# Kernel tuning notes

Measured on AMD Instinct MI355X. Metric: run time of the kernel, lower is better.

The kernel has to match this reference:

```python
import jax, jax.numpy as jnp
import numpy as np

N = 300000      # total points
B = 4           # scenes
C_IN = 64
C_OUT = 128
GRID = 0.5      # voxel size
M = 128         # per-axis voxel index bound (10m / 0.5m = 20 << 128); key fits int32
EPS = 1e-5      # BatchNorm eps


def setup_inputs() -> dict:
    key = jax.random.key(0)
    k1, k2, k3 = jax.random.split(key, 3)
    coord = jax.random.uniform(k1, (N, 3), jnp.float32) * 10.0
    feat = jax.random.normal(k2, (N, C_IN), jnp.float32)
    offset = jnp.array([N // 4, N // 2, 3 * N // 4, N], jnp.int32)  # cumulative counts
    W = jax.random.normal(k3, (C_IN, C_OUT), jnp.float32) * 0.05    # fc weight (no bias)
    gamma = jnp.ones((C_OUT,), jnp.float32)
    beta = jnp.zeros((C_OUT,), jnp.float32)
    return {"coord": coord, "feat": feat, "offset": offset, "W": W, "gamma": gamma, "beta": beta}


def reference(coord, feat, offset, W, gamma, beta):
    n = coord.shape[0]
    # offset2batch: point i belongs to scene searchsorted(offset, i, 'right')
    batch = jnp.searchsorted(offset, jnp.arange(n, dtype=offset.dtype), side='right')
    # fc -> BatchNorm1d (training-mode batch stats, biased var) -> ReLU
    x = feat @ W                                    # [n, C_OUT]
    mean = x.mean(axis=0)
    var = x.var(axis=0)
    x = jax.nn.relu(gamma * (x - mean) * jax.lax.rsqrt(var + EPS) + beta)
    # start = per-scene min coordinate (segment_csr min)
    start = jax.ops.segment_min(coord, batch, num_segments=B)      # [B, 3]
    # voxel_grid: integer voxel index per point, hashed injectively with batch id
    v = jnp.floor((coord - start[batch]) / GRID).astype(jnp.int32)  # [n, 3]
    vkey = ((batch.astype(jnp.int32) * M + v[:, 0]) * M + v[:, 1]) * M + v[:, 2]
    # unique(sorted) with inverse/counts; padded to n for static shapes
    uniq, cluster, counts = jnp.unique(vkey, return_inverse=True, return_counts=True,
                                       size=n, fill_value=-1)
    cluster = cluster.reshape(-1)                   # [n] cluster id per point
    # segment mean of coords, segment max of features (padded segments -> 0)
    cnt = jnp.maximum(counts, 1).astype(coord.dtype)
    coord_out = jax.ops.segment_sum(coord, cluster, num_segments=n) / cnt[:, None]
    fmax = jax.ops.segment_max(x, cluster, num_segments=n)
    feat_out = jnp.where(counts[:, None] > 0, fmax, jnp.zeros((), x.dtype))
    # batch id of each cluster (clusters never cross scenes)
    batch_out = jax.ops.segment_min(batch, cluster, num_segments=n)
    return coord_out, feat_out, cluster, counts, batch_out
```

## Files before the change

### kernel.cpp

```cpp
#include <hip/hip_runtime.h>
#include <stdint.h>

#define CIN   64
#define COUT  128
#define EPSB  1e-5f
#define NWORDS2 4096
#define MAXNC 32768
#define STRD  68

typedef short bf16x8 __attribute__((ext_vector_type(8)));
typedef float f32x4  __attribute__((ext_vector_type(4)));

__device__ __forceinline__ int batch_of(int i, const int* __restrict__ off, int B) {
    int b = 0;
    for (int j = 0; j < B - 1; ++j) b += (i >= off[j]) ? 1 : 0;
    return b;
}

__device__ __forceinline__ unsigned enc(float x) {
    unsigned b = __float_as_uint(x);
    return (b & 0x80000000u) ? ~b : (b | 0x80000000u);
}
__device__ __forceinline__ float dec(unsigned u) {
    unsigned b = (u & 0x80000000u) ? (u ^ 0x80000000u) : ~u;
    return __uint_as_float(b);
}

__device__ __forceinline__ unsigned short rne_bf16(float f) {
    unsigned u = __float_as_uint(f);
    unsigned r = u + 0x7FFFu + ((u >> 16) & 1u);
    return (unsigned short)(r >> 16);
}

__global__ void k_init(float* __restrict__ coordOut, float* __restrict__ batchOut, int n,
                       unsigned* __restrict__ pooledU, int* __restrict__ countsWs,
                       unsigned* __restrict__ flags, int* __restrict__ sceneMin, int nScene,
                       const float* __restrict__ W, unsigned short* __restrict__ Wb)
{
    long i = (long)blockIdx.x * blockDim.x + threadIdx.x;
    long stride = (long)gridDim.x * blockDim.x;
    for (long t = i; t < 3L * n; t += stride) coordOut[t] = 0.f;
    for (long t = i; t < n; t += stride) batchOut[t] = 2147483648.0f;
    for (long t = i; t < (long)MAXNC * COUT; t += stride) pooledU[t] = 0u;
    for (long t = i; t < MAXNC; t += stride) countsWs[t] = 0;
    for (long t = i; t < NWORDS2; t += stride) flags[t] = 0u;
    for (long t = i; t < nScene; t += stride) sceneMin[t] = 0x7F800000;
    for (long t = i; t < 32 * 64 * 8; t += stride) {
        int fragIdx = (int)(t >> 9);
        int r = (int)(t & 511);
        int lane = r >> 3, j = r & 7;
        int s  = fragIdx & 1;
        int kt = (fragIdx >> 1) & 1;
        int nt = fragIdx >> 2;
        int k  = kt * 32 + (lane >> 4) * 8 + j;
        int nc = nt * 16 + (lane & 15);
        float w = W[k * COUT + nc];
        unsigned short hi = rne_bf16(w);
        if (s == 0) Wb[t] = hi;
        else {
            float hf = __uint_as_float(((unsigned)hi) << 16);
            Wb[t] = rne_bf16(w - hf);
        }
    }
}

__global__ void k_scene_min(const float* __restrict__ coord, const int* __restrict__ off,
                            int n, int B, int* __restrict__ sceneMin)
{
    __shared__ int smin[12];
    if (threadIdx.x < 3 * B) smin[threadIdx.x] = 0x7F800000;
    __syncthreads();
    int t = blockIdx.x * blockDim.x + threadIdx.x;
    if (t < n) {
        int b = batch_of(t, off, B);
        for (int d = 0; d < 3; ++d)
            atomicMin(&smin[b * 3 + d], __float_as_int(coord[t * 3 + d]));
    }
    __syncthreads();
    if (threadIdx.x < 3 * B) atomicMin(&sceneMin[threadIdx.x], smin[threadIdx.x]);
}

__global__ void k_vkey(const float* __restrict__ coord, const int* __restrict__ off,
                       int n, int B, const int* __restrict__ sceneMin,
                       int* __restrict__ vkeyWs, unsigned* __restrict__ flags)
{
    int t = blockIdx.x * blockDim.x + threadIdx.x;
    if (t >= n) return;
    int b = batch_of(t, off, B);
    int key = b;
    #pragma unroll
    for (int d = 0; d < 3; ++d) {
        float s = __int_as_float(sceneMin[b * 3 + d]);
        int v = (int)floorf((coord[t * 3 + d] - s) * 2.0f);
        key = (key << 5) + v;
    }
    vkeyWs[t] = key;
    atomicOr(&flags[key >> 5], 1u << (key & 31));
}

__global__ void k_scan1(const unsigned* __restrict__ flags,
                        unsigned* __restrict__ wordPrefix, int* __restrict__ dNC)
{
    __shared__ unsigned wsum[16];
    const int t = threadIdx.x, lane = t & 63, wv = t >> 6;
    unsigned loc[4]; unsigned sum = 0;
    #pragma unroll
    for (int e = 0; e < 4; ++e) { loc[e] = (unsigned)__popc(flags[4 * t + e]); sum += loc[e]; }
    unsigned incl = sum;
    #pragma unroll
    for (int d = 1; d < 64; d <<= 1) {
        unsigned u = __shfl_up(incl, d, 64);
        if (lane >= d) incl += u;
    }
    if (lane == 63) wsum[wv] = incl;
    __syncthreads();
    if (wv == 0) {
        unsigned v = (lane < 16) ? wsum[lane] : 0u;
        unsigned iv = v;
        #pragma unroll
        for (int d = 1; d < 16; d <<= 1) {
            unsigned u = __shfl_up(iv, d, 64);
            if (lane >= d) iv += u;
        }
        if (lane < 16) wsum[lane] = iv - v;
    }
    __syncthreads();
    unsigned run = wsum[wv] + incl - sum;
    #pragma unroll
    for (int e = 0; e < 4; ++e) { wordPrefix[4 * t + e] = run; run += loc[e]; }
    if (t == 1023) *dNC = (int)run;
}

__global__ void k_cluster(const int* __restrict__ vkeyWs, const int* __restrict__ off,
                          int n, int B,
                          const unsigned* __restrict__ flags, const unsigned* __restrict__ wordPrefix,
                          float* __restrict__ clusterOut,
                          int* __restrict__ countsWs, float* __restrict__ batchOut)
{
    int t = blockIdx.x * blockDim.x + threadIdx.x;
    if (t >= n) return;
    int key = vkeyWs[t];
    int w = key >> 5, bit = key & 31;
    int c = (int)wordPrefix[w] + __popc(flags[w] & ((1u << bit) - 1u));
    clusterOut[t] = (float)c;
    atomicAdd(&countsWs[c], 1);
    batchOut[c] = (float)(key >> 15);
}

__global__ void k_scan2(const int* __restrict__ counts, int* __restrict__ cursor)
{
    __shared__ int wsum[16];
    const int t = threadIdx.x, lane = t & 63, wv = t >> 6;
    const int base = t * 32;
    int loc[32]; int sum = 0;
    #pragma unroll
    for (int e = 0; e < 32; ++e) { loc[e] = counts[base + e]; sum += loc[e]; }
    int incl = sum;
    #pragma unroll
    for (int d = 1; d < 64; d <<= 1) {
        int u = __shfl_up(incl, d, 64);
        if (lane >= d) incl += u;
    }
    if (lane == 63) wsum[wv] = incl;
    __syncthreads();
    if (wv == 0) {
        int v = (lane < 16) ? wsum[lane] : 0;
        int iv = v;
        #pragma unroll
        for (int d = 1; d < 16; d <<= 1) {
            int u = __shfl_up(iv, d, 64);
            if (lane >= d) iv += u;
        }
        if (lane < 16) wsum[lane] = iv - v;
    }
    __syncthreads();
    int run = wsum[wv] + incl - sum;
    #pragma unroll
    for (int e = 0; e < 32; ++e) { cursor[base + e] = run; run += loc[e]; }
}

__global__ void k_scatter(const float* __restrict__ clusterOut, int n,
                          int* __restrict__ cursor, int* __restrict__ perm,
                          int* __restrict__ sortedCid)
{
    int t = blockIdx.x * blockDim.x + threadIdx.x;
    if (t >= n) return;
    int c = (int)clusterOut[t];
    int pos = atomicAdd(&cursor[c], 1);
    perm[pos] = t;
    sortedCid[pos] = c;
}

__global__ __launch_bounds__(256, 2) void k_fused(
    const float* __restrict__ feat, const float* __restrict__ coord,
    const unsigned short* __restrict__ Wb,
    const int* __restrict__ perm, const int* __restrict__ sortedCid,
    int n, int nWin, int gFused,
    unsigned* __restrict__ pooledU, float* __restrict__ coordOut,
    float* __restrict__ partials)
{
    __shared__ float lds[4][64 * STRD];
    __shared__ float cst[4][192];
    __shared__ float accS[256];
    const int tid = threadIdx.x, wave = tid >> 6, lane = tid & 63;
    accS[tid] = 0.f;
    __syncthreads();

    const int wid = blockIdx.x * 4 + wave;
    const int q = lane >> 4, c16 = lane & 15;

    if (wid < nWin) {
        const int base = wid * 64;
        const int nvalid = min(64, n - base);
        const int pv = (lane < nvalid) ? perm[base + lane] : 0;
        const int cv = (lane < nvalid) ? sortedCid[base + lane] : -1;
        float* st = lds[wave];
        float* cs = cst[wave];

        int prevc = __shfl_up(cv, 1, 64);
        unsigned long long bmask = __ballot(lane > 0 && lane < nvalid && cv != prevc);

        for (int i0 = 0; i0 < 64; i0 += 4) {
            int idx = i0 + q;
            int p = __shfl(pv, idx, 64);
            float4 v = make_float4(0.f, 0.f, 0.f, 0.f);
            if (idx < nvalid)
                v = ((const float4*)(feat + (size_t)p * CIN))[c16];
            *(float4*)&st[idx * STRD + c16 * 4] = v;
        }
        for (int i0 = 0; i0 < 64; i0 += 16) {
            int idx = i0 + (lane >> 2);
            int d = lane & 3;
            int p = __shfl(pv, idx, 64);
            if (d < 3 && idx < nvalid) cs[idx * 3 + d] = coord[p * 3 + d];
        }

        {
            float csum = 0.f;
            int runStart = 0;
            for (int i = 0; i < nvalid; ++i) {
                if (i > 0 && ((bmask >> i) & 1ull)) {
                    int cid = __shfl(cv, i - 1, 64);
                    if (lane < 3) {
                        float* cb = coordOut + (size_t)cid * 3 + lane;
                        if (runStart == 0) atomicAdd(cb, csum);
                        else               *cb = csum;
                    }
                    runStart = i; csum = 0.f;
                }
                if (lane < 3) csum += cs[i * 3 + lane];
            }
            int cidL = __shfl(cv, nvalid - 1, 64);
            if (lane < 3) atomicAdd(coordOut + (size_t)cidL * 3 + lane, csum);
        }

        bf16x8 ahi[4][2], alo[4][2];
        #pragma unroll
        for (int mt = 0; mt < 4; ++mt) {
            #pragma unroll
            for (int kt = 0; kt < 2; ++kt) {
                int m = mt * 16 + c16;
                int k0 = kt * 32 + q * 8;
                float4 fa = *(const float4*)&st[m * STRD + k0];
                float4 fb = *(const float4*)&st[m * STRD + k0 + 4];
                float tmp[8] = { fa.x, fa.y, fa.z, fa.w, fb.x, fb.y, fb.z, fb.w };
                bf16x8 h8, l8;
                #pragma unroll
                for (int j = 0; j < 8; ++j) {
                    unsigned short h = rne_bf16(tmp[j]);
                    float hf = __uint_as_float(((unsigned)h) << 16);
                    h8[j] = (short)h;
                    l8[j] = (short)rne_bf16(tmp[j] - hf);
                }
                ahi[mt][kt] = h8;
                alo[mt][kt] = l8;
            }
        }

        for (int h = 0; h < 2; ++h) {
            bf16x8 bh[4][2], bl[4][2];
            #pragma unroll
            for (int nt2 = 0; nt2 < 4; ++nt2)
                #pragma unroll
                for (int kt = 0; kt < 2; ++kt) {
                    int fi = h * 16 + (nt2 * 2 + kt) * 2;
                    bh[nt2][kt] = *(const bf16x8*)(Wb + ((size_t)fi << 9) + (lane << 3));
                    bl[nt2][kt] = *(const bf16x8*)(Wb + ((size_t)(fi + 1) << 9) + (lane << 3));
                }
            #pragma unroll
            for (int mt = 0; mt < 4; ++mt) {
                #pragma unroll
                for (int nt2 = 0; nt2 < 4; ++nt2) {
                    f32x4 c = {0.f, 0.f, 0.f, 0.f};
                    #pragma unroll
                    for (int kt = 0; kt < 2; ++kt) {
                        c = __builtin_amdgcn_mfma_f32_16x16x32_bf16(alo[mt][kt], bh[nt2][kt], c, 0, 0, 0);
                        c = __builtin_amdgcn_mfma_f32_16x16x32_bf16(ahi[mt][kt], bl[nt2][kt], c, 0, 0, 0);
                        c = __builtin_amdgcn_mfma_f32_16x16x32_bf16(ahi[mt][kt], bh[nt2][kt], c, 0, 0, 0);
                    }
                    int col = nt2 * 16 + c16;
                    int row0 = mt * 16 + q * 4;
                    *(float4*)&st[col * STRD + row0] = make_float4(c[0], c[1], c[2], c[3]);
                }
            }
            float runM = -INFINITY, s1 = 0.f, s2 = 0.f;
            int runStart = 0;
            for (int ip = 0; ip < 16; ++ip) {
                if (ip * 4 >= nvalid) break;
                float4 v = *(const float4*)&st[lane * STRD + ip * 4];
                #pragma unroll
                for (int e = 0; e < 4; ++e) {
                    int i = ip * 4 + e;
                    if (i < nvalid) {
                        if (i > 0 && ((bmask >> i) & 1ull)) {
                            int cid = __shfl(cv, i - 1, 64);
                            unsigned* pb = pooledU + (size_t)cid * COUT + h * 64 + lane;
                            if (runStart == 0) atomicMax(pb, enc(runM));
                            else               *pb = enc(runM);
                            runStart = i;
                            runM = -INFINITY;
                        }
                        float x = (e == 0) ? v.x : (e == 1) ? v.y : (e == 2) ? v.z : v.w;
                        runM = fmaxf(runM, x);
                        s1 += x;
                        s2 = fmaf(x, x, s2);
                    }
                }
            }
            int cidL = __shfl(cv, nvalid - 1, 64);
            atomicMax(pooledU + (size_t)cidL * COUT + h * 64 + lane, enc(runM));
            atomicAdd(&accS[h * 64 + lane],       s1);
            atomicAdd(&accS[128 + h * 64 + lane], s2);
        }
    }

    __syncthreads();
    partials[(size_t)tid * gFused + blockIdx.x] = accS[tid];
}

__global__ void k_redbn(const float* __restrict__ partials, int gFused,
                        const float* __restrict__ gamma, const float* __restrict__ beta,
                        int n, float* __restrict__ scaleShift)
{
    __shared__ float red[512];
    const int j = blockIdx.x;
    const float* colS = partials + (size_t)j * gFused;
    const float* colQ = partials + (size_t)(j + 128) * gFused;
    float s = 0.f, q = 0.f;
    for (int b = threadIdx.x; b < gFused; b += 256) { s += colS[b]; q += colQ[b]; }
    red[threadIdx.x] = s;
    red[256 + threadIdx.x] = q;
    __syncthreads();
    for (int st = 128; st; st >>= 1) {
        if (threadIdx.x < st) {
            red[threadIdx.x] += red[threadIdx.x + st];
            red[256 + threadIdx.x] += red[256 + threadIdx.x + st];
        }
        __syncthreads();
    }
    if (threadIdx.x == 0) {
        float mean = red[0] / (float)n;
        float var  = red[256] / (float)n - mean * mean;
        var = fmaxf(var, 0.f);
        float inv = rsqrtf(var + EPSB);
        float sc = gamma[j] * inv;
        scaleShift[j]        = sc;
        scaleShift[COUT + j] = beta[j] - mean * sc;
    }
}

__global__ void k_final(float* __restrict__ featOut, const unsigned* __restrict__ pooledU,
                        const int* __restrict__ dNC, const float* __restrict__ scaleShift,
                        long featN4, int n,
                        float* __restrict__ coordOut, float* __restrict__ countsOut,
                        const int* __restrict__ countsWs)
{
    long i = (long)blockIdx.x * blockDim.x + threadIdx.x;
    long stride = (long)gridDim.x * blockDim.x;
    long act4 = (long)(*dNC) * (COUT / 4);
    float4* out4 = (float4*)featOut;
    const uint4* p4 = (const uint4*)pooledU;
    for (long idx = i; idx < featN4; idx += stride) {
        float4 v = make_float4(0.f, 0.f, 0.f, 0.f);
        if (idx < act4) {
            int j = (int)((idx * 4) & (COUT - 1));
            uint4 u = p4[idx];
            v.x = fmaxf(fmaf(scaleShift[j + 0], dec(u.x), scaleShift[COUT + j + 0]), 0.f);
            v.y = fmaxf(fmaf(scaleShift[j + 1], dec(u.y), scaleShift[COUT + j + 1]), 0.f);
            v.z = fmaxf(fmaf(scaleShift[j + 2], dec(u.z), scaleShift[COUT + j + 2]), 0.f);
            v.w = fmaxf(fmaf(scaleShift[j + 3], dec(u.w), scaleShift[COUT + j + 3]), 0.f);
        }
        out4[idx] = v;
    }
    for (long t = i; t < n; t += stride) {
        int cnt = (t < MAXNC) ? countsWs[t] : 0;
        if (cnt > 0) {
            float inv = 1.f / (float)cnt;
            coordOut[3 * t + 0] *= inv;
            coordOut[3 * t + 1] *= inv;
            coordOut[3 * t + 2] *= inv;
        }
        countsOut[t] = (float)cnt;
    }
}

extern "C" void kernel_launch(void* const* d_in, const int* in_sizes, int n_in,
                              void* d_out, int out_size, void* d_ws, size_t ws_size,
                              hipStream_t stream)
{
    const float* coord = (const float*)d_in[0];
    const float* feat  = (const float*)d_in[1];
    const int*   off   = (const int*)d_in[2];
    const float* W     = (const float*)d_in[3];
    const float* gamma = (const float*)d_in[4];
    const float* beta  = (const float*)d_in[5];
    const int n = in_sizes[0] / 3;
    const int B = in_sizes[2];

    float* out        = (float*)d_out;
    float* coordOut   = out;
    float* featOut    = out + (long)n * 3;
    float* clusterOut = featOut + (long)n * COUT;
    float* countsOut  = clusterOut + n;
    float* batchOut   = countsOut + n;

    char* wsp = (char*)d_ws;
    auto alloc = [&](size_t bytes) -> char* {
        char* p = wsp;
        wsp += (bytes + 255) & ~(size_t)255;
        return p;
    };
    unsigned* flags      = (unsigned*)alloc(NWORDS2 * 4);
    unsigned* wordPrefix = (unsigned*)alloc(NWORDS2 * 4);
    int*      vkeyWs     = (int*)alloc((size_t)n * 4);
    int*      countsWs   = (int*)alloc(MAXNC * 4);
    int*      perm       = (int*)alloc((size_t)n * 4);
    int*      sortedCid  = (int*)alloc((size_t)n * 4);
    int*      cursor     = (int*)alloc(MAXNC * 4);
    unsigned* pooledU    = (unsigned*)alloc((size_t)MAXNC * COUT * 4);
    unsigned short* Wb   = (unsigned short*)alloc(32 * 64 * 8 * 2);
    float*    scaleShift = (float*)alloc(2 * COUT * 4);
    int*      sceneMin   = (int*)alloc(3 * B * 4);
    int*      dNC        = (int*)alloc(4);

    const int nWin = (n + 63) / 64;
    const int gFused = (nWin + 3) / 4;
    float*    partials   = (float*)alloc((size_t)gFused * 256 * 4);

    const long featN4 = (long)n * COUT / 4;
    const int nb = (n + 255) / 256;

    k_init<<<nb, 256, 0, stream>>>(coordOut, batchOut, n, pooledU, countsWs,
                                   flags, sceneMin, 3 * B, W, Wb);
    k_scene_min<<<nb, 256, 0, stream>>>(coord, off, n, B, sceneMin);
    k_vkey<<<nb, 256, 0, stream>>>(coord, off, n, B, sceneMin, vkeyWs, flags);
    k_scan1<<<1, 1024, 0, stream>>>(flags, wordPrefix, dNC);
    k_cluster<<<nb, 256, 0, stream>>>(vkeyWs, off, n, B, flags, wordPrefix,
                                      clusterOut, countsWs, batchOut);
    k_scan2<<<1, 1024, 0, stream>>>(countsWs, cursor);
    k_scatter<<<nb, 256, 0, stream>>>(clusterOut, n, cursor, perm, sortedCid);
    k_fused<<<gFused, 256, 0, stream>>>(feat, coord, Wb, perm, sortedCid, n, nWin, gFused,
                                        pooledU, coordOut, partials);
    k_redbn<<<128, 256, 0, stream>>>(partials, gFused, gamma, beta, n, scaleShift);
    k_final<<<2048, 256, 0, stream>>>(featOut, pooledU, dNC, scaleShift, featN4, n,
                                      coordOut, countsOut, countsWs);
}
```

Measured before the change: 418.1 us.

## Rework fused pooling kernel with persistent work-stealing waves and smaller LDS

```diff
diff --git a/kernel.cpp b/kernel.cpp
--- a/kernel.cpp
+++ b/kernel.cpp
@@ -6,10 +6,10 @@
 #define EPSB  1e-5f
 #define NWORDS2 4096
 #define MAXNC 32768
-#define STRD  68
 
 typedef short bf16x8 __attribute__((ext_vector_type(8)));
 typedef float f32x4  __attribute__((ext_vector_type(4)));
+typedef unsigned u32x4 __attribute__((ext_vector_type(4)));
 
 __device__ __forceinline__ int batch_of(int i, const int* __restrict__ off, int B) {
     int b = 0;
@@ -32,13 +32,31 @@
     return (unsigned short)(r >> 16);
 }
 
+__device__ __forceinline__ void split8(float4 A, float4 B, bf16x8& hi, bf16x8& lo) {
+    float fs[8] = {A.x, A.y, A.z, A.w, B.x, B.y, B.z, B.w};
+    u32x4 hv, lv;
+    #pragma unroll
+    for (int w = 0; w < 4; ++w) {
+        float a = fs[2*w], b = fs[2*w+1];
+        unsigned ua = __float_as_uint(a), ub = __float_as_uint(b);
+        hv[w] = __builtin_amdgcn_perm(ub, ua, 0x07060302u);
+        float la = a - __uint_as_float(ua & 0xFFFF0000u);
+        float lb = b - __uint_as_float(ub & 0xFFFF0000u);
+        lv[w] = __builtin_amdgcn_perm(__float_as_uint(lb), __float_as_uint(la), 0x07060302u);
+    }
+    hi = __builtin_bit_cast(bf16x8, hv);
+    lo = __builtin_bit_cast(bf16x8, lv);
+}
+
 __global__ void k_init(float* __restrict__ coordOut, float* __restrict__ batchOut, int n,
                        unsigned* __restrict__ pooledU, int* __restrict__ countsWs,
                        unsigned* __restrict__ flags, int* __restrict__ sceneMin, int nScene,
-                       const float* __restrict__ W, unsigned short* __restrict__ Wb)
+                       const float* __restrict__ W, unsigned short* __restrict__ Wb,
+                       int* __restrict__ wCtr)
 {
     long i = (long)blockIdx.x * blockDim.x + threadIdx.x;
     long stride = (long)gridDim.x * blockDim.x;
+    if (i == 0) *wCtr = 0;
     for (long t = i; t < 3L * n; t += stride) coordOut[t] = 0.f;
     for (long t = i; t < n; t += stride) batchOut[t] = 2147483648.0f;
     for (long t = i; t < (long)MAXNC * COUT; t += stride) pooledU[t] = 0u;
@@ -180,158 +198,159 @@
 }
 
 __global__ void k_scatter(const float* __restrict__ clusterOut, int n,
-                          int* __restrict__ cursor, int* __restrict__ perm,
-                          int* __restrict__ sortedCid)
+                          int* __restrict__ cursor, int2* __restrict__ pcPair)
 {
     int t = blockIdx.x * blockDim.x + threadIdx.x;
     if (t >= n) return;
     int c = (int)clusterOut[t];
     int pos = atomicAdd(&cursor[c], 1);
-    perm[pos] = t;
-    sortedCid[pos] = c;
-}
-
-__global__ __launch_bounds__(256, 2) void k_fused(
+    pcPair[pos] = make_int2(t, c);
+}
+
+template<bool FULL>
+__device__ __forceinline__ void do_window(
+    int wid, int n, const float* __restrict__ feat, const float* __restrict__ coord,
+    const unsigned short* __restrict__ Wb, const int2* __restrict__ pc,
+    unsigned* __restrict__ pooledU, float* __restrict__ coordOut,
+    float* __restrict__ accS, float* __restrict__ slab, int lane)
+{
+    const int q = lane >> 4, c16 = lane & 15;
+    const int base = wid * 64;
+    const int nvalid = FULL ? 64 : (n - base);
+
+    int pv = 0, cv = -1;
+    if (FULL || lane < nvalid) { int2 t = pc[base + lane]; pv = t.x; cv = t.y; }
+    int prevc = __shfl_up(cv, 1, 64);
+    unsigned long long bmask = __ballot(lane > 0 && (FULL || lane < nvalid) && cv != prevc);
+
+    {
+        float cx = 0.f, cy = 0.f, cz = 0.f;
+        if (FULL || lane < nvalid) {
+            const float* cp = coord + 3 * (size_t)pv;
+            cx = cp[0]; cy = cp[1]; cz = cp[2];
+        }
+        unsigned long long mlow = bmask & (~0ull >> (63 - lane));
+        int rs = mlow ? (63 - __clzll((long long)mlow)) : 0;
+        #pragma unroll
+        for (int d = 1; d < 64; d <<= 1) {
+            float tx = __shfl_up(cx, d, 64);
+            float ty = __shfl_up(cy, d, 64);
+            float tz = __shfl_up(cz, d, 64);
+            if (lane - rs >= d) { cx += tx; cy += ty; cz += tz; }
+        }
+        bool isEnd = (lane == nvalid - 1) || ((((bmask >> 1) >> lane) & 1ull) != 0ull);
+        if ((FULL || lane < nvalid) && isEnd) {
+            float* cb = coordOut + (size_t)cv * 3;
+            if (rs == 0 || lane == nvalid - 1) {
+                atomicAdd(cb + 0, cx); atomicAdd(cb + 1, cy); atomicAdd(cb + 2, cz);
+            } else {
+                cb[0] = cx; cb[1] = cy; cb[2] = cz;
+            }
+        }
+    }
+
+    bf16x8 ahi[4][2], alo[4][2];
+    #pragma unroll
+    for (int mt = 0; mt < 4; ++mt) {
+        int m = mt * 16 + c16;
+        int p = __shfl(pv, m, 64);
+        const float* ap = feat + (size_t)p * CIN + q * 8;
+        #pragma unroll
+        for (int kt = 0; kt < 2; ++kt) {
+            float4 fa = make_float4(0.f, 0.f, 0.f, 0.f), fb = fa;
+            if (FULL || m < nvalid) {
+                fa = *(const float4*)(ap + kt * 32);
+                fb = *(const float4*)(ap + kt * 32 + 4);
+            }
+            split8(fa, fb, ahi[mt][kt], alo[mt][kt]);
+        }
+    }
+
+    const int rk = (lane >> 3) & 3;
+    int rdOff[4], wOff[4];
+    #pragma unroll
+    for (int g = 0; g < 4; ++g) rdOff[g] = lane * 20 + (((g ^ rk) & 3) << 2);
+    #pragma unroll
+    for (int t2 = 0; t2 < 4; ++t2) {
+        int col = t2 * 16 + c16;
+        wOff[t2] = col * 20 + (((q ^ ((col >> 3) & 3)) & 3) << 2);
+    }
+
+    const unsigned short* wb = Wb + (lane << 3);
+
+    #pragma unroll 1
+    for (int h = 0; h < 2; ++h) {
+        float runM = -__builtin_inff(), s1 = 0.f, s2 = 0.f;
+        int runStart = 0;
+        #pragma unroll
+        for (int mt = 0; mt < 4; ++mt) {
+            #pragma unroll
+            for (int t2 = 0; t2 < 4; ++t2) {
+                int fi = h * 16 + t2 * 4;
+                bf16x8 bh0 = *(const bf16x8*)(wb + ((size_t)(fi + 0) << 9));
+                bf16x8 bl0 = *(const bf16x8*)(wb + ((size_t)(fi + 1) << 9));
+                bf16x8 bh1 = *(const bf16x8*)(wb + ((size_t)(fi + 2) << 9));
+                bf16x8 bl1 = *(const bf16x8*)(wb + ((size_t)(fi + 3) << 9));
+                f32x4 c = {0.f, 0.f, 0.f, 0.f};
+                c = __builtin_amdgcn_mfma_f32_16x16x32_bf16(alo[mt][0], bh0, c, 0, 0, 0);
+                c = __builtin_amdgcn_mfma_f32_16x16x32_bf16(ahi[mt][0], bl0, c, 0, 0, 0);
+                c = __builtin_amdgcn_mfma_f32_16x16x32_bf16(ahi[mt][0], bh0, c, 0, 0, 0);
+                c = __builtin_amdgcn_mfma_f32_16x16x32_bf16(alo[mt][1], bh1, c, 0, 0, 0);
+                c = __builtin_amdgcn_mfma_f32_16x16x32_bf16(ahi[mt][1], bl1, c, 0, 0, 0);
+                c = __builtin_amdgcn_mfma_f32_16x16x32_bf16(ahi[mt][1], bh1, c, 0, 0, 0);
+                *(float4*)&slab[wOff[t2]] = make_float4(c[0], c[1], c[2], c[3]);
+            }
+            #pragma unroll
+            for (int g = 0; g < 4; ++g) {
+                float4 v = *(const float4*)&slab[rdOff[g]];
+                #pragma unroll
+                for (int e = 0; e < 4; ++e) {
+                    const int i = mt * 16 + g * 4 + e;
+                    if (i > 0 && ((bmask >> i) & 1ull)) {
+                        int pcid = __shfl(cv, i - 1, 64);
+                        unsigned* pb = pooledU + (size_t)pcid * COUT + h * 64 + lane;
+                        if (runStart == 0) atomicMax(pb, enc(runM));
+                        else               *pb = enc(runM);
+                        runStart = i;
+                        runM = -__builtin_inff();
+                    }
+                    float x = (e == 0) ? v.x : (e == 1) ? v.y : (e == 2) ? v.z : v.w;
+                    if (FULL || i < nvalid) runM = fmaxf(runM, x);
+                    s1 += x;
+                    s2 = fmaf(x, x, s2);
+                }
+            }
+        }
+        int cidL = __shfl(cv, nvalid - 1, 64);
+        atomicMax(pooledU + (size_t)cidL * COUT + h * 64 + lane, enc(runM));
+        atomicAdd(&accS[h * 64 + lane],       s1);
+        atomicAdd(&accS[128 + h * 64 + lane], s2);
+    }
+}
+
+__global__ __launch_bounds__(256, 4) void k_fused(
     const float* __restrict__ feat, const float* __restrict__ coord,
-    const unsigned short* __restrict__ Wb,
-    const int* __restrict__ perm, const int* __restrict__ sortedCid,
-    int n, int nWin, int gFused,
+    const unsigned short* __restrict__ Wb, const int2* __restrict__ pc,
+    int n, int nWin, int gFused, int* __restrict__ wCtr,
     unsigned* __restrict__ pooledU, float* __restrict__ coordOut,
     float* __restrict__ partials)
 {
-    __shared__ float lds[4][64 * STRD];
-    __shared__ float cst[4][192];
+    __shared__ float slabs[4][64 * 20];
     __shared__ float accS[256];
     const int tid = threadIdx.x, wave = tid >> 6, lane = tid & 63;
     accS[tid] = 0.f;
     __syncthreads();
-
-    const int wid = blockIdx.x * 4 + wave;
-    const int q = lane >> 4, c16 = lane & 15;
-
-    if (wid < nWin) {
-        const int base = wid * 64;
-        const int nvalid = min(64, n - base);
-        const int pv = (lane < nvalid) ? perm[base + lane] : 0;
-        const int cv = (lane < nvalid) ? sortedCid[base + lane] : -1;
-        float* st = lds[wave];
-        float* cs = cst[wave];
-
-        int prevc = __shfl_up(cv, 1, 64);
-        unsigned long long bmask = __ballot(lane > 0 && lane < nvalid && cv != prevc);
-
-        for (int i0 = 0; i0 < 64; i0 += 4) {
-            int idx = i0 + q;
-            int p = __shfl(pv, idx, 64);
-            float4 v = make_float4(0.f, 0.f, 0.f, 0.f);
-            if (idx < nvalid)
-                v = ((const float4*)(feat + (size_t)p * CIN))[c16];
-            *(float4*)&st[idx * STRD + c16 * 4] = v;
-        }
-        for (int i0 = 0; i0 < 64; i0 += 16) {
-            int idx = i0 + (lane >> 2);
-            int d = lane & 3;
-            int p = __shfl(pv, idx, 64);
-            if (d < 3 && idx < nvalid) cs[idx * 3 + d] = coord[p * 3 + d];
-        }
-
-        {
-            float csum = 0.f;
-            int runStart = 0;
-            for (int i = 0; i < nvalid; ++i) {
-                if (i > 0 && ((bmask >> i) & 1ull)) {
-                    int cid = __shfl(cv, i - 1, 64);
-                    if (lane < 3) {
-                        float* cb = coordOut + (size_t)cid * 3 + lane;
-                        if (runStart == 0) atomicAdd(cb, csum);
-                        else               *cb = csum;
-                    }
-                    runStart = i; csum = 0.f;
-                }
-                if (lane < 3) csum += cs[i * 3 + lane];
-            }
-            int cidL = __shfl(cv, nvalid - 1, 64);
-            if (lane < 3) atomicAdd(coordOut + (size_t)cidL * 3 + lane, csum);
-        }
-
-        bf16x8 ahi[4][2], alo[4][2];
-        #pragma unroll
-        for (int mt = 0; mt < 4; ++mt) {
-            #pragma unroll
-            for (int kt = 0; kt < 2; ++kt) {
-                int m = mt * 16 + c16;
-                int k0 = kt * 32 + q * 8;
-                float4 fa = *(const float4*)&st[m * STRD + k0];
-                float4 fb = *(const float4*)&st[m * STRD + k0 + 4];
-                float tmp[8] = { fa.x, fa.y, fa.z, fa.w, fb.x, fb.y, fb.z, fb.w };
-                bf16x8 h8, l8;
-                #pragma unroll
-                for (int j = 0; j < 8; ++j) {
-                    unsigned short h = rne_bf16(tmp[j]);
-                    float hf = __uint_as_float(((unsigned)h) << 16);
-                    h8[j] = (short)h;
-                    l8[j] = (short)rne_bf16(tmp[j] - hf);
-                }
-                ahi[mt][kt] = h8;
-                alo[mt][kt] = l8;
-            }
-        }
-
-        for (int h = 0; h < 2; ++h) {
-            bf16x8 bh[4][2], bl[4][2];
-            #pragma unroll
-            for (int nt2 = 0; nt2 < 4; ++nt2)
-                #pragma unroll
-                for (int kt = 0; kt < 2; ++kt) {
-                    int fi = h * 16 + (nt2 * 2 + kt) * 2;
-                    bh[nt2][kt] = *(const bf16x8*)(Wb + ((size_t)fi << 9) + (lane << 3));
-                    bl[nt2][kt] = *(const bf16x8*)(Wb + ((size_t)(fi + 1) << 9) + (lane << 3));
-                }
-            #pragma unroll
-            for (int mt = 0; mt < 4; ++mt) {
-                #pragma unroll
-                for (int nt2 = 0; nt2 < 4; ++nt2) {
-                    f32x4 c = {0.f, 0.f, 0.f, 0.f};
-                    #pragma unroll
-                    for (int kt = 0; kt < 2; ++kt) {
-                        c = __builtin_amdgcn_mfma_f32_16x16x32_bf16(alo[mt][kt], bh[nt2][kt], c, 0, 0, 0);
-                        c = __builtin_amdgcn_mfma_f32_16x16x32_bf16(ahi[mt][kt], bl[nt2][kt], c, 0, 0, 0);
-                        c = __builtin_amdgcn_mfma_f32_16x16x32_bf16(ahi[mt][kt], bh[nt2][kt], c, 0, 0, 0);
-                    }
-                    int col = nt2 * 16 + c16;
-                    int row0 = mt * 16 + q * 4;
-                    *(float4*)&st[col * STRD + row0] = make_float4(c[0], c[1], c[2], c[3]);
-                }
-            }
-            float runM = -INFINITY, s1 = 0.f, s2 = 0.f;
-            int runStart = 0;
-            for (int ip = 0; ip < 16; ++ip) {
-                if (ip * 4 >= nvalid) break;
-                float4 v = *(const float4*)&st[lane * STRD + ip * 4];
-                #pragma unroll
-                for (int e = 0; e < 4; ++e) {
-                    int i = ip * 4 + e;
-                    if (i < nvalid) {
-                        if (i > 0 && ((bmask >> i) & 1ull)) {
-                            int cid = __shfl(cv, i - 1, 64);
-                            unsigned* pb = pooledU + (size_t)cid * COUT + h * 64 + lane;
-                            if (runStart == 0) atomicMax(pb, enc(runM));
-                            else               *pb = enc(runM);
-                            runStart = i;
-                            runM = -INFINITY;
-                        }
-                        float x = (e == 0) ? v.x : (e == 1) ? v.y : (e == 2) ? v.z : v.w;
-                        runM = fmaxf(runM, x);
-                        s1 += x;
-                        s2 = fmaf(x, x, s2);
-                    }
-                }
-            }
-            int cidL = __shfl(cv, nvalid - 1, 64);
-            atomicMax(pooledU + (size_t)cidL * COUT + h * 64 + lane, enc(runM));
-            atomicAdd(&accS[h * 64 + lane],       s1);
-            atomicAdd(&accS[128 + h * 64 + lane], s2);
-        }
+    float* slab = slabs[wave];
+
+    for (;;) {
+        int w = 0;
+        if (lane == 0) w = atomicAdd(wCtr, 1);
+        w = __shfl(w, 0, 64);
+        if (w >= nWin) break;
+        if (w < nWin - 1)
+            do_window<true >(w, n, feat, coord, Wb, pc, pooledU, coordOut, accS, slab, lane);
+        else
+            do_window<false>(w, n, feat, coord, Wb, pc, pooledU, coordOut, accS, slab, lane);
     }
 
     __syncthreads();
@@ -434,32 +453,32 @@
     unsigned* wordPrefix = (unsigned*)alloc(NWORDS2 * 4);
     int*      vkeyWs     = (int*)alloc((size_t)n * 4);
     int*      countsWs   = (int*)alloc(MAXNC * 4);
-    int*      perm       = (int*)alloc((size_t)n * 4);
-    int*      sortedCid  = (int*)alloc((size_t)n * 4);
+    int2*     pcPair     = (int2*)alloc((size_t)n * sizeof(int2));
     int*      cursor     = (int*)alloc(MAXNC * 4);
     unsigned* pooledU    = (unsigned*)alloc((size_t)MAXNC * COUT * 4);
     unsigned short* Wb   = (unsigned short*)alloc(32 * 64 * 8 * 2);
     float*    scaleShift = (float*)alloc(2 * COUT * 4);
     int*      sceneMin   = (int*)alloc(3 * B * 4);
     int*      dNC        = (int*)alloc(4);
+    int*      wCtr       = (int*)alloc(4);
 
     const int nWin = (n + 63) / 64;
-    const int gFused = (nWin + 3) / 4;
+    const int gFused = 1024;
     float*    partials   = (float*)alloc((size_t)gFused * 256 * 4);
 
     const long featN4 = (long)n * COUT / 4;
     const int nb = (n + 255) / 256;
 
     k_init<<<nb, 256, 0, stream>>>(coordOut, batchOut, n, pooledU, countsWs,
-                                   flags, sceneMin, 3 * B, W, Wb);
+                                   flags, sceneMin, 3 * B, W, Wb, wCtr);
     k_scene_min<<<nb, 256, 0, stream>>>(coord, off, n, B, sceneMin);
     k_vkey<<<nb, 256, 0, stream>>>(coord, off, n, B, sceneMin, vkeyWs, flags);
     k_scan1<<<1, 1024, 0, stream>>>(flags, wordPrefix, dNC);
     k_cluster<<<nb, 256, 0, stream>>>(vkeyWs, off, n, B, flags, wordPrefix,
                                       clusterOut, countsWs, batchOut);
     k_scan2<<<1, 1024, 0, stream>>>(countsWs, cursor);
-    k_scatter<<<nb, 256, 0, stream>>>(clusterOut, n, cursor, perm, sortedCid);
-    k_fused<<<gFused, 256, 0, stream>>>(feat, coord, Wb, perm, sortedCid, n, nWin, gFused,
+    k_scatter<<<nb, 256, 0, stream>>>(clusterOut, n, cursor, pcPair);
+    k_fused<<<gFused, 256, 0, stream>>>(feat, coord, Wb, pcPair, n, nWin, gFused, wCtr,
                                         pooledU, coordOut, partials);
     k_redbn<<<128, 256, 0, stream>>>(partials, gFused, gamma, beta, n, scaleShift);
     k_final<<<2048, 256, 0, stream>>>(featOut, pooledU, dNC, scaleShift, featN4, n,
```

Result: slower. 519.0 us (+24.1%).

## Halve fused-kernel LDS staging, pack perm/cluster pairs, cheapen bf16 split

Applied to the files above, without the earlier changes.

```diff
diff --git a/kernel.cpp b/kernel.cpp
--- a/kernel.cpp
+++ b/kernel.cpp
@@ -6,10 +6,12 @@
 #define EPSB  1e-5f
 #define NWORDS2 4096
 #define MAXNC 32768
-#define STRD  68
+#define STGS  68
+#define SLABW 17
 
 typedef short bf16x8 __attribute__((ext_vector_type(8)));
 typedef float f32x4  __attribute__((ext_vector_type(4)));
+typedef unsigned u32x4 __attribute__((ext_vector_type(4)));
 
 __device__ __forceinline__ int batch_of(int i, const int* __restrict__ off, int B) {
     int b = 0;
@@ -30,6 +32,22 @@
     unsigned u = __float_as_uint(f);
     unsigned r = u + 0x7FFFu + ((u >> 16) & 1u);
     return (unsigned short)(r >> 16);
+}
+
+__device__ __forceinline__ void split8(float4 A, float4 B, bf16x8& hi, bf16x8& lo) {
+    float fs[8] = {A.x, A.y, A.z, A.w, B.x, B.y, B.z, B.w};
+    u32x4 hv, lv;
+    #pragma unroll
+    for (int w = 0; w < 4; ++w) {
+        float a = fs[2*w], b = fs[2*w+1];
+        unsigned ua = __float_as_uint(a), ub = __float_as_uint(b);
+        hv[w] = __builtin_amdgcn_perm(ub, ua, 0x07060302u);
+        float la = a - __uint_as_float(ua & 0xFFFF0000u);
+        float lb = b - __uint_as_float(ub & 0xFFFF0000u);
+        lv[w] = __builtin_amdgcn_perm(__float_as_uint(lb), __float_as_uint(la), 0x07060302u);
+    }
+    hi = __builtin_bit_cast(bf16x8, hv);
+    lo = __builtin_bit_cast(bf16x8, lv);
 }
 
 __global__ void k_init(float* __restrict__ coordOut, float* __restrict__ batchOut, int n,
@@ -180,26 +198,23 @@
 }
 
 __global__ void k_scatter(const float* __restrict__ clusterOut, int n,
-                          int* __restrict__ cursor, int* __restrict__ perm,
-                          int* __restrict__ sortedCid)
+                          int* __restrict__ cursor, int2* __restrict__ pcPair)
 {
     int t = blockIdx.x * blockDim.x + threadIdx.x;
     if (t >= n) return;
     int c = (int)clusterOut[t];
     int pos = atomicAdd(&cursor[c], 1);
-    perm[pos] = t;
-    sortedCid[pos] = c;
+    pcPair[pos] = make_int2(t, c);
 }
 
 __global__ __launch_bounds__(256, 2) void k_fused(
     const float* __restrict__ feat, const float* __restrict__ coord,
-    const unsigned short* __restrict__ Wb,
-    const int* __restrict__ perm, const int* __restrict__ sortedCid,
+    const unsigned short* __restrict__ Wb, const int2* __restrict__ pc,
     int n, int nWin, int gFused,
     unsigned* __restrict__ pooledU, float* __restrict__ coordOut,
     float* __restrict__ partials)
 {
-    __shared__ float lds[4][64 * STRD];
+    __shared__ float stg[4][32 * STGS];
     __shared__ float cst[4][192];
     __shared__ float accS[256];
     const int tid = threadIdx.x, wave = tid >> 6, lane = tid & 63;
@@ -212,22 +227,14 @@
     if (wid < nWin) {
         const int base = wid * 64;
         const int nvalid = min(64, n - base);
-        const int pv = (lane < nvalid) ? perm[base + lane] : 0;
-        const int cv = (lane < nvalid) ? sortedCid[base + lane] : -1;
-        float* st = lds[wave];
+        int pv = 0, cv = -1;
+        if (lane < nvalid) { int2 t = pc[base + lane]; pv = t.x; cv = t.y; }
+        float* st = stg[wave];
         float* cs = cst[wave];
 
         int prevc = __shfl_up(cv, 1, 64);
         unsigned long long bmask = __ballot(lane > 0 && lane < nvalid && cv != prevc);
 
-        for (int i0 = 0; i0 < 64; i0 += 4) {
-            int idx = i0 + q;
-            int p = __shfl(pv, idx, 64);
-            float4 v = make_float4(0.f, 0.f, 0.f, 0.f);
-            if (idx < nvalid)
-                v = ((const float4*)(feat + (size_t)p * CIN))[c16];
-            *(float4*)&st[idx * STRD + c16 * 4] = v;
-        }
         for (int i0 = 0; i0 < 64; i0 += 16) {
             int idx = i0 + (lane >> 2);
             int d = lane & 3;
@@ -255,25 +262,28 @@
         }
 
         bf16x8 ahi[4][2], alo[4][2];
-        #pragma unroll
-        for (int mt = 0; mt < 4; ++mt) {
+        #pragma unroll 1
+        for (int ph = 0; ph < 2; ++ph) {
             #pragma unroll
-            for (int kt = 0; kt < 2; ++kt) {
-                int m = mt * 16 + c16;
-                int k0 = kt * 32 + q * 8;
-                float4 fa = *(const float4*)&st[m * STRD + k0];
-                float4 fb = *(const float4*)&st[m * STRD + k0 + 4];
-                float tmp[8] = { fa.x, fa.y, fa.z, fa.w, fb.x, fb.y, fb.z, fb.w };
-                bf16x8 h8, l8;
+            for (int i0 = 0; i0 < 32; i0 += 4) {
+                int idx = i0 + q;
+                int gi  = ph * 32 + idx;
+                int p = __shfl(pv, gi, 64);
+                float4 v = make_float4(0.f, 0.f, 0.f, 0.f);
+                if (gi < nvalid)
+                    v = ((const float4*)(feat + (size_t)p * CIN))[c16];
+                *(float4*)&st[idx * STGS + c16 * 4] = v;
+            }
+            #pragma unroll
+            for (int mh = 0; mh < 2; ++mh) {
+                int mt = ph * 2 + mh;
+                int lr = mh * 16 + c16;
                 #pragma unroll
-                for (int j = 0; j < 8; ++j) {
-                    unsigned short h = rne_bf16(tmp[j]);
-                    float hf = __uint_as_float(((unsigned)h) << 16);
-                    h8[j] = (short)h;
-                    l8[j] = (short)rne_bf16(tmp[j] - hf);
+                for (int kt = 0; kt < 2; ++kt) {
+                    float4 fa = *(const float4*)&st[lr * STGS + kt * 32 + q * 8];
+                    float4 fb = *(const float4*)&st[lr * STGS + kt * 32 + q * 8 + 4];
+                    split8(fa, fb, ahi[mt][kt], alo[mt][kt]);
                 }
-                ahi[mt][kt] = h8;
-                alo[mt][kt] = l8;
             }
         }
 
@@ -300,14 +310,14 @@
                     }
                     int col = nt2 * 16 + c16;
                     int row0 = mt * 16 + q * 4;
-                    *(float4*)&st[col * STRD + row0] = make_float4(c[0], c[1], c[2], c[3]);
+                    *(float4*)&st[col * SLABW + row0] = make_float4(c[0], c[1], c[2], c[3]);
                 }
             }
-            float runM = -INFINITY, s1 = 0.f, s2 = 0.f;
+            float runM = -__builtin_inff(), s1 = 0.f, s2 = 0.f;
             int runStart = 0;
             for (int ip = 0; ip < 16; ++ip) {
                 if (ip * 4 >= nvalid) break;
-                float4 v = *(const float4*)&st[lane * STRD + ip * 4];
+                float4 v = *(const float4*)&st[lane * SLABW + ip * 4];
                 #pragma unroll
                 for (int e = 0; e < 4; ++e) {
                     int i = ip * 4 + e;
@@ -318,7 +328,7 @@
                             if (runStart == 0) atomicMax(pb, enc(runM));
                             else               *pb = enc(runM);
                             runStart = i;
-                            runM = -INFINITY;
+                            runM = -__builtin_inff();
                         }
                         float x = (e == 0) ? v.x : (e == 1) ? v.y : (e == 2) ? v.z : v.w;
                         runM = fmaxf(runM, x);
@@ -434,8 +444,7 @@
     unsigned* wordPrefix = (unsigned*)alloc(NWORDS2 * 4);
     int*      vkeyWs     = (int*)alloc((size_t)n * 4);
     int*      countsWs   = (int*)alloc(MAXNC * 4);
-    int*      perm       = (int*)alloc((size_t)n * 4);
-    int*      sortedCid  = (int*)alloc((size_t)n * 4);
+    int2*     pcPair     = (int2*)alloc((size_t)n * sizeof(int2));
     int*      cursor     = (int*)alloc(MAXNC * 4);
     unsigned* pooledU    = (unsigned*)alloc((size_t)MAXNC * COUT * 4);
     unsigned short* Wb   = (unsigned short*)alloc(32 * 64 * 8 * 2);
@@ -458,8 +467,8 @@
     k_cluster<<<nb, 256, 0, stream>>>(vkeyWs, off, n, B, flags, wordPrefix,
                                       clusterOut, countsWs, batchOut);
     k_scan2<<<1, 1024, 0, stream>>>(countsWs, cursor);
-    k_scatter<<<nb, 256, 0, stream>>>(clusterOut, n, cursor, perm, sortedCid);
-    k_fused<<<gFused, 256, 0, stream>>>(feat, coord, Wb, perm, sortedCid, n, nWin, gFused,
+    k_scatter<<<nb, 256, 0, stream>>>(clusterOut, n, cursor, pcPair);
+    k_fused<<<gFused, 256, 0, stream>>>(feat, coord, Wb, pcPair, n, nWin, gFused,
                                         pooledU, coordOut, partials);
     k_redbn<<<128, 256, 0, stream>>>(partials, gFused, gamma, beta, n, scaleShift);
     k_final<<<2048, 256, 0, stream>>>(featOut, pooledU, dNC, scaleShift, featN4, n,
```

Result: slower. 530.0 us (+26.8%).
